# Kernel optimization log

Measured on AMD Instinct MI355X. Metric: run time of the kernel, lower is better.

The kernel has to match this reference:

```python
import jax, jax.numpy as jnp
import numpy as np

WINDOW_SIZE = 5  # hardcoded in module __init__


def local_window_mask(T, dtype=jnp.float32):
    # Faithful to torch code: start from triu(ones, diagonal=1) (value 1.0 for
    # j > i, NOT -inf!), then set entries outside the band |j - i| <= sz to -inf.
    sz = WINDOW_SIZE // 2
    i = jnp.arange(T)[:, None]
    j = jnp.arange(T)[None, :]
    upper = (j > i).astype(dtype)            # triu part contributes +1 bias
    in_band = jnp.abs(j - i) <= sz
    return jnp.where(in_band, upper, jnp.float32(-jnp.inf).astype(dtype))


def setup_inputs() -> dict:
    key = jax.random.key(0)
    kx, kq, kk, kv = jax.random.split(key, 4)
    B, T, C = 4, 4096, 64
    head_size = 64
    s = 1.0 / np.sqrt(C)
    return {
        "x": jax.random.normal(kx, (B, T, C), dtype=jnp.float32),
        "Wq": jax.random.normal(kq, (head_size, C), dtype=jnp.float32) * s,
        "Wk": jax.random.normal(kk, (head_size, C), dtype=jnp.float32) * s,
        "Wv": jax.random.normal(kv, (head_size, C), dtype=jnp.float32) * s,
    }


def reference(x, Wq, Wk, Wv):
    B, T, C = x.shape
    # nn.Linear(d_model, head_size, bias=False): y = x @ W.T
    q = jnp.einsum('btc,hc->bth', x, Wq)
    k = jnp.einsum('btc,hc->bth', x, Wk)
    v = jnp.einsum('btc,hc->bth', x, Wv)
    scale = jnp.asarray(C, x.dtype) ** -0.5   # scale uses input dim C
    scores = jnp.einsum('bth,bsh->bts', q, k) * scale + local_window_mask(T, x.dtype)
    attn = jax.nn.softmax(scores, axis=-1)    # original computes this twice; once suffices (same math)
    op = jnp.einsum('bts,bsh->bth', attn, v)
    return (op, attn)
```

## Files before the change

### kernel.cpp

```cpp
#include <hip/hip_runtime.h>

constexpr int B      = 4;
constexpr int T      = 4096;
constexpr int C      = 64;
constexpr int H      = 64;
constexpr int TILE   = 32;
constexpr int HALO   = 2;
constexpr int HR     = TILE + 2 * HALO;
constexpr int LS     = 68;
constexpr int NT     = 256;
constexpr int NTILES = T / TILE;
constexpr int CBLOCKS = B * NTILES;
constexpr int T4     = T / 4;

__global__ __launch_bounds__(NT, 2)
void sparse_attn_fused(const float* __restrict__ x,
                       const float* __restrict__ Wq,
                       const float* __restrict__ Wk,
                       const float* __restrict__ Wv,
                       float* __restrict__ out)
{
    __shared__ float sX[HR][LS];
    __shared__ float sW[C][LS];
    __shared__ float sU[TILE][LS];
    __shared__ float sS[TILE][8];

    const int tid = threadIdx.x;
    const size_t attnBase = (size_t)B * T * H;

    const int b    = (int)(blockIdx.x / NTILES);
    const int tile = (int)(blockIdx.x % NTILES);
    const int row0 = tile * TILE;
    const float* xb = x + (size_t)b * T * C;

    for (int s = tid; s < HR * (C / 4); s += NT) {
        const int lr = s >> 4;
        const int c4 = (s & 15) << 2;
        const int gr = row0 + lr - HALO;
        float4 v = make_float4(0.f, 0.f, 0.f, 0.f);
        if (gr >= 0 && gr < T) v = *(const float4*)(xb + (size_t)gr * C + c4);
        *(float4*)&sX[lr][c4] = v;
    }
    {
        const int c   = tid >> 2;
        const int cp0 = (tid & 3) << 4;
        float acc[16];
#pragma unroll
        for (int j = 0; j < 16; ++j) acc[j] = 0.f;
#pragma unroll 4
        for (int h = 0; h < C; ++h) {
            const float  wq = Wq[h * 64 + c];
            const float4 k0 = *(const float4*)&Wk[h * 64 + cp0];
            const float4 k1 = *(const float4*)&Wk[h * 64 + cp0 + 4];
            const float4 k2 = *(const float4*)&Wk[h * 64 + cp0 + 8];
            const float4 k3 = *(const float4*)&Wk[h * 64 + cp0 + 12];
            acc[0]  = fmaf(wq, k0.x, acc[0]);  acc[1]  = fmaf(wq, k0.y, acc[1]);
            acc[2]  = fmaf(wq, k0.z, acc[2]);  acc[3]  = fmaf(wq, k0.w, acc[3]);
            acc[4]  = fmaf(wq, k1.x, acc[4]);  acc[5]  = fmaf(wq, k1.y, acc[5]);
            acc[6]  = fmaf(wq, k1.z, acc[6]);  acc[7]  = fmaf(wq, k1.w, acc[7]);
            acc[8]  = fmaf(wq, k2.x, acc[8]);  acc[9]  = fmaf(wq, k2.y, acc[9]);
            acc[10] = fmaf(wq, k2.z, acc[10]); acc[11] = fmaf(wq, k2.w, acc[11]);
            acc[12] = fmaf(wq, k3.x, acc[12]); acc[13] = fmaf(wq, k3.y, acc[13]);
            acc[14] = fmaf(wq, k3.z, acc[14]); acc[15] = fmaf(wq, k3.w, acc[15]);
        }
#pragma unroll
        for (int j = 0; j < 4; ++j)
            *(float4*)&sW[c][cp0 + 4 * j] =
                make_float4(acc[4*j], acc[4*j+1], acc[4*j+2], acc[4*j+3]);
    }
    __syncthreads();

    {
        const int r0 = tid >> 4;
        const int h0 = (tid & 15) << 2;
        float acc[2][4];
#pragma unroll
        for (int k = 0; k < 2; ++k)
#pragma unroll
            for (int j = 0; j < 4; ++j) acc[k][j] = 0.f;
        for (int c4 = 0; c4 < C; c4 += 4) {
            const float4 xa = *(const float4*)&sX[r0 + HALO][c4];
            const float4 xc = *(const float4*)&sX[r0 + 16 + HALO][c4];
#pragma unroll
            for (int cc = 0; cc < 4; ++cc) {
                const float4 wv = *(const float4*)&sW[c4 + cc][h0];
                const float xs0 = (&xa.x)[cc];
                const float xs1 = (&xc.x)[cc];
                acc[0][0] = fmaf(xs0, wv.x, acc[0][0]);
                acc[0][1] = fmaf(xs0, wv.y, acc[0][1]);
                acc[0][2] = fmaf(xs0, wv.z, acc[0][2]);
                acc[0][3] = fmaf(xs0, wv.w, acc[0][3]);
                acc[1][0] = fmaf(xs1, wv.x, acc[1][0]);
                acc[1][1] = fmaf(xs1, wv.y, acc[1][1]);
                acc[1][2] = fmaf(xs1, wv.z, acc[1][2]);
                acc[1][3] = fmaf(xs1, wv.w, acc[1][3]);
            }
        }
        *(float4*)&sU[r0][h0]      = make_float4(acc[0][0], acc[0][1], acc[0][2], acc[0][3]);
        *(float4*)&sU[r0 + 16][h0] = make_float4(acc[1][0], acc[1][1], acc[1][2], acc[1][3]);
    }
    __syncthreads();

    if (tid < TILE) {
        const int i  = tid;
        const int ig = row0 + i;
        float sc[5];
        float m = -__builtin_inff();
#pragma unroll
        for (int d = 0; d < 5; ++d) {
            const int jg = ig - HALO + d;
            float v = -__builtin_inff();
            if (jg >= 0 && jg < T) {
                float a = 0.f;
#pragma unroll
                for (int c4 = 0; c4 < C; c4 += 4) {
                    const float4 u  = *(const float4*)&sU[i][c4];
                    const float4 xk = *(const float4*)&sX[i + d][c4];
                    a += u.x * xk.x + u.y * xk.y + u.z * xk.z + u.w * xk.w;
                }
                v = a * 0.125f + (d > 2 ? 1.0f : 0.0f);
            }
            sc[d] = v;
            m = fmaxf(m, v);
        }
        float p[5];
        float sum = 0.f;
#pragma unroll
        for (int d = 0; d < 5; ++d) { p[d] = expf(sc[d] - m); sum += p[d]; }
        const float inv = 1.f / sum;
#pragma unroll
        for (int d = 0; d < 5; ++d) sS[i][d] = p[d] * inv;
    }
    if (tid >= 64) {
        for (int s = tid - 64; s < C * H; s += NT - 64)
            sW[s & 63][s >> 6] = Wv[s];
    }
    __syncthreads();

    {
        const int i  = tid >> 3;
        const int c0 = (tid & 7) << 3;
        float y[8];
#pragma unroll
        for (int j = 0; j < 8; ++j) y[j] = 0.f;
#pragma unroll
        for (int d = 0; d < 5; ++d) {
            const float pd = sS[i][d];
            const float4 a  = *(const float4*)&sX[i + d][c0];
            const float4 b2 = *(const float4*)&sX[i + d][c0 + 4];
            y[0] = fmaf(pd, a.x, y[0]);  y[1] = fmaf(pd, a.y, y[1]);
            y[2] = fmaf(pd, a.z, y[2]);  y[3] = fmaf(pd, a.w, y[3]);
            y[4] = fmaf(pd, b2.x, y[4]); y[5] = fmaf(pd, b2.y, y[5]);
            y[6] = fmaf(pd, b2.z, y[6]); y[7] = fmaf(pd, b2.w, y[7]);
        }
        *(float4*)&sU[i][c0]     = make_float4(y[0], y[1], y[2], y[3]);
        *(float4*)&sU[i][c0 + 4] = make_float4(y[4], y[5], y[6], y[7]);
    }
    __syncthreads();

    {
        const int r0 = tid >> 4;
        const int h0 = (tid & 15) << 2;
        float acc[2][4];
#pragma unroll
        for (int k = 0; k < 2; ++k)
#pragma unroll
            for (int j = 0; j < 4; ++j) acc[k][j] = 0.f;
        for (int c4 = 0; c4 < C; c4 += 4) {
            const float4 ya = *(const float4*)&sU[r0][c4];
            const float4 yc = *(const float4*)&sU[r0 + 16][c4];
#pragma unroll
            for (int cc = 0; cc < 4; ++cc) {
                const float4 wv = *(const float4*)&sW[c4 + cc][h0];
                const float ys0 = (&ya.x)[cc];
                const float ys1 = (&yc.x)[cc];
                acc[0][0] = fmaf(ys0, wv.x, acc[0][0]);
                acc[0][1] = fmaf(ys0, wv.y, acc[0][1]);
                acc[0][2] = fmaf(ys0, wv.z, acc[0][2]);
                acc[0][3] = fmaf(ys0, wv.w, acc[0][3]);
                acc[1][0] = fmaf(ys1, wv.x, acc[1][0]);
                acc[1][1] = fmaf(ys1, wv.y, acc[1][1]);
                acc[1][2] = fmaf(ys1, wv.z, acc[1][2]);
                acc[1][3] = fmaf(ys1, wv.w, acc[1][3]);
            }
        }
        float* o = out + ((size_t)b * T + row0) * H;
        *(float4*)&o[(size_t)r0 * H + h0] =
            make_float4(acc[0][0], acc[0][1], acc[0][2], acc[0][3]);
        *(float4*)&o[(size_t)(r0 + 16) * H + h0] =
            make_float4(acc[1][0], acc[1][1], acc[1][2], acc[1][3]);
    }

    {
        float4* __restrict__ p =
            (float4*)(out + attnBase) + ((size_t)b * T + row0) * T4 + tid;
        const float4 z = make_float4(0.f, 0.f, 0.f, 0.f);
#pragma unroll 8
        for (int k = 0; k < TILE * T4 / NT; ++k)
            p[(size_t)k * NT] = z;
    }
    __syncthreads();

    if (tid < TILE) {
        const int i  = tid;
        const int ig = row0 + i;
        float* rowp = out + attnBase + ((size_t)b * T + ig) * T;
        const int cLo = (ig - HALO > 0 ? ig - HALO : 0) >> 2;
        const int cHi = (ig + HALO < T - 1 ? ig + HALO : T - 1) >> 2;
        for (int cch = cLo; cch <= cHi; ++cch) {
            float vv[4];
#pragma unroll
            for (int q = 0; q < 4; ++q) {
                const int d = (cch << 2) + q - (ig - HALO);
                vv[q] = (d >= 0 && d < 5) ? sS[i][d] : 0.f;
            }
            *(float4*)(rowp + (cch << 2)) = make_float4(vv[0], vv[1], vv[2], vv[3]);
        }
    }
}

extern "C" void kernel_launch(void* const* d_in, const int* in_sizes, int n_in,
                              void* d_out, int out_size, void* d_ws, size_t ws_size,
                              hipStream_t stream) {
    (void)in_sizes; (void)n_in; (void)d_ws; (void)ws_size; (void)out_size;
    const float* x  = (const float*)d_in[0];
    const float* Wq = (const float*)d_in[1];
    const float* Wk = (const float*)d_in[2];
    const float* Wv = (const float*)d_in[3];
    float* out = (float*)d_out;
    sparse_attn_fused<<<dim3(CBLOCKS), dim3(NT), 0, stream>>>(x, Wq, Wk, Wv, out);
}
```

Measured before the change: 295.1 us.

## Issue attn zero-fill early with nontemporal stores and LDS-only barriers

```diff
diff --git a/kernel.cpp b/kernel.cpp
--- a/kernel.cpp
+++ b/kernel.cpp
@@ -11,7 +11,14 @@
 constexpr int NT     = 256;
 constexpr int NTILES = T / TILE;
 constexpr int CBLOCKS = B * NTILES;
-constexpr int T4     = T / 4;
+
+typedef float f32x4 __attribute__((ext_vector_type(4)));
+
+__device__ __forceinline__ void lgkm_barrier() {
+    asm volatile("s_waitcnt lgkmcnt(0)" ::: "memory");
+    __builtin_amdgcn_s_barrier();
+    asm volatile("" ::: "memory");
+}
 
 __global__ __launch_bounds__(NT, 2)
 void sparse_attn_fused(const float* __restrict__ x,
@@ -20,10 +27,11 @@
                        const float* __restrict__ Wv,
                        float* __restrict__ out)
 {
-    __shared__ float sX[HR][LS];
-    __shared__ float sW[C][LS];
-    __shared__ float sU[TILE][LS];
-    __shared__ float sS[TILE][8];
+    __shared__ float sX [HR][LS];
+    __shared__ float sW [C][LS];
+    __shared__ float sWv[C][LS];
+    __shared__ float sU [TILE][LS];
+    __shared__ float sS [TILE][8];
 
     const int tid = threadIdx.x;
     const size_t attnBase = (size_t)B * T * H;
@@ -68,7 +76,24 @@
             *(float4*)&sW[c][cp0 + 4 * j] =
                 make_float4(acc[4*j], acc[4*j+1], acc[4*j+2], acc[4*j+3]);
     }
-    __syncthreads();
+    for (int s = tid; s < C * H; s += NT) sWv[s & 63][s >> 6] = Wv[s];
+
+    lgkm_barrier();
+
+    {
+        f32x4* __restrict__ attn4 = (f32x4*)(out + attnBase);
+        const size_t blkChunk = ((size_t)b * T + row0) << 10;
+        const f32x4 z = {0.f, 0.f, 0.f, 0.f};
+#pragma unroll 4
+        for (int k = 0; k < TILE * (T / 4) / NT; ++k) {
+            const int n  = (k << 8) + tid;
+            const int i  = n >> 10;
+            const int j0 = (n & 1023) << 2;
+            const int ig = row0 + i;
+            if (j0 > ig + HALO || j0 + 3 < ig - HALO)
+                __builtin_nontemporal_store(z, &attn4[blkChunk + n]);
+        }
+    }
 
     {
         const int r0 = tid >> 4;
@@ -99,7 +124,7 @@
         *(float4*)&sU[r0][h0]      = make_float4(acc[0][0], acc[0][1], acc[0][2], acc[0][3]);
         *(float4*)&sU[r0 + 16][h0] = make_float4(acc[1][0], acc[1][1], acc[1][2], acc[1][3]);
     }
-    __syncthreads();
+    lgkm_barrier();
 
     if (tid < TILE) {
         const int i  = tid;
@@ -130,12 +155,21 @@
         const float inv = 1.f / sum;
 #pragma unroll
         for (int d = 0; d < 5; ++d) sS[i][d] = p[d] * inv;
-    }
-    if (tid >= 64) {
-        for (int s = tid - 64; s < C * H; s += NT - 64)
-            sW[s & 63][s >> 6] = Wv[s];
-    }
-    __syncthreads();
+
+        float* rowp = out + attnBase + ((size_t)b * T + ig) * T;
+        const int cLo = (ig - HALO > 0 ? ig - HALO : 0) >> 2;
+        const int cHi = (ig + HALO < T - 1 ? ig + HALO : T - 1) >> 2;
+        for (int cch = cLo; cch <= cHi; ++cch) {
+            float vv[4];
+#pragma unroll
+            for (int q = 0; q < 4; ++q) {
+                const int d = (cch << 2) + q - (ig - HALO);
+                vv[q] = (d >= 0 && d < 5) ? sS[i][d] : 0.f;
+            }
+            *(float4*)(rowp + (cch << 2)) = make_float4(vv[0], vv[1], vv[2], vv[3]);
+        }
+    }
+    lgkm_barrier();
 
     {
         const int i  = tid >> 3;
@@ -156,7 +190,7 @@
         *(float4*)&sU[i][c0]     = make_float4(y[0], y[1], y[2], y[3]);
         *(float4*)&sU[i][c0 + 4] = make_float4(y[4], y[5], y[6], y[7]);
     }
-    __syncthreads();
+    lgkm_barrier();
 
     {
         const int r0 = tid >> 4;
@@ -171,7 +205,7 @@
             const float4 yc = *(const float4*)&sU[r0 + 16][c4];
 #pragma unroll
             for (int cc = 0; cc < 4; ++cc) {
-                const float4 wv = *(const float4*)&sW[c4 + cc][h0];
+                const float4 wv = *(const float4*)&sWv[c4 + cc][h0];
                 const float ys0 = (&ya.x)[cc];
                 const float ys1 = (&yc.x)[cc];
                 acc[0][0] = fmaf(ys0, wv.x, acc[0][0]);
@@ -189,33 +223,6 @@
             make_float4(acc[0][0], acc[0][1], acc[0][2], acc[0][3]);
         *(float4*)&o[(size_t)(r0 + 16) * H + h0] =
             make_float4(acc[1][0], acc[1][1], acc[1][2], acc[1][3]);
-    }
-
-    {
-        float4* __restrict__ p =
-            (float4*)(out + attnBase) + ((size_t)b * T + row0) * T4 + tid;
-        const float4 z = make_float4(0.f, 0.f, 0.f, 0.f);
-#pragma unroll 8
-        for (int k = 0; k < TILE * T4 / NT; ++k)
-            p[(size_t)k * NT] = z;
-    }
-    __syncthreads();
-
-    if (tid < TILE) {
-        const int i  = tid;
-        const int ig = row0 + i;
-        float* rowp = out + attnBase + ((size_t)b * T + ig) * T;
-        const int cLo = (ig - HALO > 0 ? ig - HALO : 0) >> 2;
-        const int cHi = (ig + HALO < T - 1 ? ig + HALO : T - 1) >> 2;
-        for (int cch = cLo; cch <= cHi; ++cch) {
-            float vv[4];
-#pragma unroll
-            for (int q = 0; q < 4; ++q) {
-                const int d = (cch << 2) + q - (ig - HALO);
-                vv[q] = (d >= 0 && d < 5) ? sS[i][d] : 0.f;
-            }
-            *(float4*)(rowp + (cch << 2)) = make_float4(vv[0], vv[1], vv[2], vv[3]);
-        }
     }
 }
 
```

New measurement: 319.0 us. +8.1%, slower.
